# Optimization experiments

Measured on AMD Instinct MI355X. Metric: run time of the kernel, lower is better.

## Reference

```python
import jax, jax.numpy as jnp
import numpy as np

B, A, F, D, C = 256, 128, 512, 6, 512  # batch, max_atoms, atom_features, max_degree, conv_width


def setup_inputs() -> dict:
    key = jax.random.key(0)
    k1, k2, k3, k4 = jax.random.split(key, 4)
    atoms = jax.random.normal(k1, (B, A, F), dtype=jnp.float32)
    # neighbour indices in [0, A); pad entries beyond each atom's degree with -1
    neigh = jax.random.randint(k2, (B, A, D), 0, A)
    deg = jax.random.randint(k3, (B, A, 1), 0, D)  # degrees in 0..D-1
    bonds = jnp.where(jnp.arange(D)[None, None, :] < deg, neigh, -1)
    # one Dense(conv_width) per degree: stacked kernels [D, F, C] and biases [D, C]
    W = jax.random.normal(k4, (D, F, C), dtype=jnp.float32) * 0.02
    b = jnp.zeros((D, C), dtype=jnp.float32)
    return {"atoms": atoms, "bonds": bonds, "W": W, "b": b}


def reference(atoms, bonds, W, b):
    d_max = bonds.shape[-1]
    # per-atom degree = count of non -1 neighbour slots  [B, A, 1]
    degrees = jnp.sum(bonds != -1, axis=-1, keepdims=True)
    # shift lookup by 1 so that padded (-1) neighbours index a zero row
    padded = jnp.pad(atoms, ((0, 0), (1, 1), (0, 0)))  # [B, A+2, F]
    idx = bonds + 1  # [B, A, D]
    # per-sample gather of neighbour features -> [B, A, D, F]
    neigh_feats = jax.vmap(lambda ref, i: ref[i])(padded, idx)
    summed = jnp.sum(neigh_feats, axis=2) + atoms  # [B, A, F]
    # apply all degree-specific dense layers, then mask-select by degree
    dense = jnp.einsum('baf,dfc->badc', summed, W) + b  # [B, A, D, C]
    masks = (degrees[..., None] == jnp.arange(d_max).reshape(1, 1, d_max, 1)).astype(dense.dtype)
    return jnp.sum(dense * masks, axis=2)  # [B, A, C]
```

## Files before the change

kernel.cpp:

```cpp
#include <hip/hip_runtime.h>
#include <hip/hip_bf16.h>


#define NB 256
#define NA 128
#define NF 512
#define ND 6
#define NC 512
#define NATOMS (NB * NA)

typedef __attribute__((ext_vector_type(8))) short frag8;
typedef __attribute__((ext_vector_type(4))) float f32x4;

static __device__ inline unsigned short f2bu(float f) {
    __hip_bfloat16 h = __float2bfloat16(f);
    return *reinterpret_cast<unsigned short*>(&h);
}
static __device__ inline unsigned int pack2(float a, float b) {
    return (unsigned int)f2bu(a) | ((unsigned int)f2bu(b) << 16);
}

__global__ void transpose_w(const float* __restrict__ W,
                            __hip_bfloat16* __restrict__ Wt) {
    __shared__ float t[32][33];
    const int d  = blockIdx.z;
    const int c0 = blockIdx.x * 32;
    const int f0 = blockIdx.y * 32;
    #pragma unroll
    for (int r = 0; r < 32; r += 8)
        t[threadIdx.y + r][threadIdx.x] =
            W[((size_t)(d * NF + f0 + threadIdx.y + r)) * NC + c0 + threadIdx.x];
    __syncthreads();
    #pragma unroll
    for (int r = 0; r < 32; r += 8)
        Wt[((size_t)(d * NC + c0 + threadIdx.y + r)) * NF + f0 + threadIdx.x] =
            __float2bfloat16(t[threadIdx.x][threadIdx.y + r]);
}

__global__ __launch_bounds__(256) void bucket_atoms(
    const int* __restrict__ bonds, int* __restrict__ counts,
    int* __restrict__ bucket) {
    __shared__ int lcnt[ND];
    __shared__ int lbase[ND];
    const int tid = threadIdx.x;
    if (tid < ND) lcnt[tid] = 0;
    __syncthreads();
    int deg[4], loc[4], gg[4];
    #pragma unroll
    for (int i = 0; i < 4; ++i) {
        int g = blockIdx.x * 1024 + i * 256 + tid;
        gg[i] = g;
        int dg = 0;
        #pragma unroll
        for (int j = 0; j < ND; ++j) dg += (bonds[g * ND + j] >= 0);
        deg[i] = dg;
        loc[i] = atomicAdd(&lcnt[dg], 1);
    }
    __syncthreads();
    if (tid < ND) lbase[tid] = atomicAdd(&counts[tid], lcnt[tid]);
    __syncthreads();
    #pragma unroll
    for (int i = 0; i < 4; ++i)
        bucket[deg[i] * NATOMS + lbase[deg[i]] + loc[i]] = gg[i];
}

__global__ __launch_bounds__(256) void sum_neigh(
    const float* __restrict__ atoms, const int* __restrict__ bonds,
    __hip_bfloat16* __restrict__ summed) {
    const int tid  = threadIdx.x;
    const int wave = tid >> 6;
    const int lane = tid & 63;
    const int g    = blockIdx.x * 4 + wave;
    const float4* a4 = (const float4*)atoms;

    int   nb[ND];
    float msk[ND];
    #pragma unroll
    for (int j = 0; j < ND; ++j) {
        int n = bonds[g * ND + j];
        msk[j] = (n >= 0) ? 1.0f : 0.0f;
        nb[j]  = (n >= 0) ? n : 0;
    }
    const int rowbase = g & ~(NA - 1);

    float4 s0 = a4[(size_t)g * 128 + lane];
    float4 s1 = a4[(size_t)g * 128 + 64 + lane];
    float4 v0[ND], v1[ND];
    #pragma unroll
    for (int j = 0; j < ND; ++j) {
        const size_t base = (size_t)(rowbase + nb[j]) * 128;
        v0[j] = a4[base + lane];
        v1[j] = a4[base + 64 + lane];
    }
    #pragma unroll
    for (int j = 0; j < ND; ++j) {
        s0.x = fmaf(v0[j].x, msk[j], s0.x); s0.y = fmaf(v0[j].y, msk[j], s0.y);
        s0.z = fmaf(v0[j].z, msk[j], s0.z); s0.w = fmaf(v0[j].w, msk[j], s0.w);
        s1.x = fmaf(v1[j].x, msk[j], s1.x); s1.y = fmaf(v1[j].y, msk[j], s1.y);
        s1.z = fmaf(v1[j].z, msk[j], s1.z); s1.w = fmaf(v1[j].w, msk[j], s1.w);
    }

    uint2 o0, o1;
    o0.x = pack2(s0.x, s0.y); o0.y = pack2(s0.z, s0.w);
    o1.x = pack2(s1.x, s1.y); o1.y = pack2(s1.z, s1.w);
    ((uint2*)summed)[(size_t)g * 128 + lane] = o0;
    ((uint2*)summed)[(size_t)g * 128 + 64 + lane] = o1;
}

__global__ __launch_bounds__(256, 2) void gemm_deg(
    const __hip_bfloat16* __restrict__ summed, const __hip_bfloat16* __restrict__ Wt,
    const float* __restrict__ bias, const int* __restrict__ counts,
    const int* __restrict__ bucket, float* __restrict__ out) {
    const int d  = blockIdx.z;
    const int Md = counts[d];
    const int m0 = blockIdx.x * 128;
    if (m0 >= Md) return;
    const int n0 = blockIdx.y * 128;

    __shared__ __align__(16) __hip_bfloat16 sA[128 * 64];
    __shared__ __align__(16) __hip_bfloat16 sB[128 * 64];
    __shared__ int sRows[128];

    const int tid = threadIdx.x;
    if (tid < 128) {
        int r = m0 + tid;
        sRows[tid] = (r < Md) ? bucket[d * NATOMS + r] : -1;
    }
    __syncthreads();

    const int seg     = tid & 7;
    const int baseRow = tid >> 3;
    int gr[4];
    #pragma unroll
    for (int r = 0; r < 4; ++r) {
        int q = sRows[baseRow + 32 * r];
        gr[r] = (q < 0) ? 0 : q;
    }

    const int lane = tid & 63;
    const int w    = tid >> 6;
    const int wy = w >> 1, wx = w & 1;
    const int quad = lane >> 4, l16 = lane & 15;

    f32x4 acc[4][4];
    #pragma unroll
    for (int i = 0; i < 4; ++i)
        #pragma unroll
        for (int j = 0; j < 4; ++j) acc[i][j] = (f32x4)0.0f;

    uint4* sA4 = (uint4*)sA;
    uint4* sB4 = (uint4*)sB;
    const uint4* sm4 = (const uint4*)summed;
    const uint4* wt4 = (const uint4*)Wt;

    for (int kt = 0; kt < NF / 64; ++kt) {
        const int k8 = kt * 8;
        #pragma unroll
        for (int r = 0; r < 4; ++r) {
            const int row = baseRow + 32 * r;
            sA4[row * 8 + seg] = sm4[(size_t)gr[r] * 64 + k8 + seg];
            sB4[row * 8 + seg] = wt4[(size_t)(d * NC + n0 + row) * 64 + k8 + seg];
        }
        __syncthreads();
        #pragma unroll
        for (int ks = 0; ks < 64; ks += 32) {
            frag8 aF[4], bF[4];
            #pragma unroll
            for (int i = 0; i < 4; ++i)
                aF[i] = *(const frag8*)&sA[(wy * 64 + i * 16 + l16) * 64 + ks + quad * 8];
            #pragma unroll
            for (int j = 0; j < 4; ++j)
                bF[j] = *(const frag8*)&sB[(wx * 64 + j * 16 + l16) * 64 + ks + quad * 8];
            #pragma unroll
            for (int i = 0; i < 4; ++i)
                #pragma unroll
                for (int j = 0; j < 4; ++j)
                    acc[i][j] = __builtin_amdgcn_mfma_f32_16x16x32_bf16(
                        aF[i], bF[j], acc[i][j], 0, 0, 0);
        }
        __syncthreads();
    }

    #pragma unroll
    for (int j = 0; j < 4; ++j) {
        const int n = n0 + wx * 64 + j * 16 + l16;
        const float bv = bias[d * NC + n];
        #pragma unroll
        for (int i = 0; i < 4; ++i) {
            #pragma unroll
            for (int r = 0; r < 4; ++r) {
                const int tr = wy * 64 + i * 16 + quad * 4 + r;
                const int g  = sRows[tr];
                if (g >= 0)
                    out[(size_t)g * NC + n] = acc[i][j][r] + bv;
            }
        }
    }
}

extern "C" void kernel_launch(void* const* d_in, const int* in_sizes, int n_in,
                              void* d_out, int out_size, void* d_ws, size_t ws_size,
                              hipStream_t stream) {
    const float* atoms = (const float*)d_in[0];
    const int*   bonds = (const int*)d_in[1];
    const float* W     = (const float*)d_in[2];
    const float* bias  = (const float*)d_in[3];
    float* out = (float*)d_out;

    char* ws = (char*)d_ws;
    int* counts = (int*)ws;
    int* bucket = (int*)(ws + 1024);
    __hip_bfloat16* Wt     = (__hip_bfloat16*)(ws + 1024 + 786432);
    __hip_bfloat16* summed = (__hip_bfloat16*)(ws + 1024 + 786432 + 3145728);

    hipMemsetAsync(counts, 0, 1024, stream);

    transpose_w<<<dim3(NC / 32, NF / 32, ND), dim3(32, 8), 0, stream>>>(W, Wt);

    bucket_atoms<<<NATOMS / 1024, 256, 0, stream>>>(bonds, counts, bucket);

    sum_neigh<<<NATOMS / 4, 256, 0, stream>>>(atoms, bonds, summed);

    gemm_deg<<<dim3(NATOMS / 128, NC / 128, ND), 256, 0, stream>>>(
        summed, Wt, bias, counts, bucket, out);
}
```

Before: 196.0 us.

## Load GEMM tiles with direct global-to-LDS async loads and reorder grid

Replaces the register-staged global-to-shared copies in the degree-bucketed GEMM with global_load_lds 16-byte direct-to-LDS loads, so tile fills no longer pass through VGPRs. The grid is remapped so degree and N-tile share the x dimension, putting blocks with the same M tile adjacent in launch order to improve reuse of gathered rows in cache. Launch bounds are raised to allow 4 blocks per CU. The tile loop still has no double buffering, and correctness depends on the implicit wait before the barrier covering the async LDS writes.

```diff
diff --git a/kernel.cpp b/kernel.cpp
--- a/kernel.cpp
+++ b/kernel.cpp
@@ -18,6 +18,11 @@
 }
 static __device__ inline unsigned int pack2(float a, float b) {
     return (unsigned int)f2bu(a) | ((unsigned int)f2bu(b) << 16);
+}
+static __device__ inline void async16(const void* g, void* l) {
+    __builtin_amdgcn_global_load_lds(
+        (const __attribute__((address_space(1))) void*)g,
+        (__attribute__((address_space(3))) void*)l, 16, 0, 0);
 }
 
 __global__ void transpose_w(const float* __restrict__ W,
@@ -107,15 +112,16 @@
     ((uint2*)summed)[(size_t)g * 128 + 64 + lane] = o1;
 }
 
-__global__ __launch_bounds__(256, 2) void gemm_deg(
+__global__ __launch_bounds__(256, 4) void gemm_deg(
     const __hip_bfloat16* __restrict__ summed, const __hip_bfloat16* __restrict__ Wt,
     const float* __restrict__ bias, const int* __restrict__ counts,
     const int* __restrict__ bucket, float* __restrict__ out) {
-    const int d  = blockIdx.z;
+    const int bx = blockIdx.x;
+    const int d  = bx % ND;
+    const int n0 = (bx / ND) * 128;
     const int Md = counts[d];
-    const int m0 = blockIdx.x * 128;
+    const int m0 = blockIdx.y * 128;
     if (m0 >= Md) return;
-    const int n0 = blockIdx.y * 128;
 
     __shared__ __align__(16) __hip_bfloat16 sA[128 * 64];
     __shared__ __align__(16) __hip_bfloat16 sB[128 * 64];
@@ -128,19 +134,24 @@
     }
     __syncthreads();
 
-    const int seg     = tid & 7;
-    const int baseRow = tid >> 3;
-    int gr[4];
-    #pragma unroll
-    for (int r = 0; r < 4; ++r) {
-        int q = sRows[baseRow + 32 * r];
-        gr[r] = (q < 0) ? 0 : q;
-    }
-
     const int lane = tid & 63;
     const int w    = tid >> 6;
+    const int srow = lane >> 3;
+    const int seg  = lane & 7;
+
+    const char* smB = (const char*)summed;
+    const char* wtB = (const char*)Wt + (size_t)(d * NC + n0) * (NF * 2);
+    size_t gA[4];
+    int    rowc[4];
+    #pragma unroll
+    for (int c = 0; c < 4; ++c) {
+        rowc[c] = w * 32 + c * 8 + srow;
+        int q = sRows[rowc[c]];
+        gA[c] = (size_t)((q < 0) ? 0 : q) * (NF * 2);
+    }
+
+    const int quad = lane >> 4, l16 = lane & 15;
     const int wy = w >> 1, wx = w & 1;
-    const int quad = lane >> 4, l16 = lane & 15;
 
     f32x4 acc[4][4];
     #pragma unroll
@@ -148,18 +159,12 @@
         #pragma unroll
         for (int j = 0; j < 4; ++j) acc[i][j] = (f32x4)0.0f;
 
-    uint4* sA4 = (uint4*)sA;
-    uint4* sB4 = (uint4*)sB;
-    const uint4* sm4 = (const uint4*)summed;
-    const uint4* wt4 = (const uint4*)Wt;
-
     for (int kt = 0; kt < NF / 64; ++kt) {
-        const int k8 = kt * 8;
-        #pragma unroll
-        for (int r = 0; r < 4; ++r) {
-            const int row = baseRow + 32 * r;
-            sA4[row * 8 + seg] = sm4[(size_t)gr[r] * 64 + k8 + seg];
-            sB4[row * 8 + seg] = wt4[(size_t)(d * NC + n0 + row) * 64 + k8 + seg];
+        const int koff = kt * 128 + seg * 16;
+        #pragma unroll
+        for (int c = 0; c < 4; ++c) {
+            async16(smB + gA[c] + koff, &sA[(w * 32 + c * 8) * 64]);
+            async16(wtB + (size_t)rowc[c] * (NF * 2) + koff, &sB[(w * 32 + c * 8) * 64]);
         }
         __syncthreads();
         #pragma unroll
@@ -221,6 +226,6 @@
 
     sum_neigh<<<NATOMS / 4, 256, 0, stream>>>(atoms, bonds, summed);
 
-    gemm_deg<<<dim3(NATOMS / 128, NC / 128, ND), 256, 0, stream>>>(
+    gemm_deg<<<dim3(24, NATOMS / 128), 256, 0, stream>>>(
         summed, Wt, bias, counts, bucket, out);
 }
```

Result: faster. 184.2 us (-6.0%).
